# Optimization experiments

Hardware: AMD Instinct MI355X
Metric: run time of the kernel (lower is better)

## Reference

```python
import jax, jax.numpy as jnp
import numpy as np

B, S, D = 4, 2048, 1024
H, HD = 16, 64
DFF = 4096
EPS = 1e-6


def setup_inputs() -> dict:
    key = jax.random.key(0)
    ks = jax.random.split(key, 16)
    sc = 0.02
    def w(k, shape):
        return jax.random.normal(k, shape, dtype=jnp.float32) * sc
    return {
        'x': jax.random.normal(ks[0], (B, S, D), dtype=jnp.float32),
        'wq': w(ks[1], (D, D)), 'bq': jnp.zeros((D,), jnp.float32),
        'wk': w(ks[2], (D, D)), 'bk': jnp.zeros((D,), jnp.float32),
        'wv': w(ks[3], (D, D)), 'bv': jnp.zeros((D,), jnp.float32),
        'wo': w(ks[4], (D, D)), 'bo': jnp.zeros((D,), jnp.float32),
        'w1': w(ks[5], (D, DFF)), 'b1': jnp.zeros((DFF,), jnp.float32),
        'w2': w(ks[6], (DFF, D)), 'b2': jnp.zeros((D,), jnp.float32),
        'ln1_a': jnp.ones((D,), jnp.float32), 'ln1_b': jnp.zeros((D,), jnp.float32),
        'ln2_a': jnp.ones((D,), jnp.float32), 'ln2_b': jnp.zeros((D,), jnp.float32),
    }


def layernorm(x, alpha, bias):
    # Matches torch module: std is unbiased (ddof=1), divide by (std + eps)
    mean = jnp.mean(x, axis=-1, keepdims=True)
    var = jnp.sum((x - mean) ** 2, axis=-1, keepdims=True) / (x.shape[-1] - 1)
    std = jnp.sqrt(var)
    return alpha * ((x - mean) / (std + EPS)) + bias


def mha(x, wq, bq, wk, bk, wv, bv, wo, bo):
    q = (x @ wq + bq).reshape(B, S, H, HD)
    k = (x @ wk + bk).reshape(B, S, H, HD)
    v = (x @ wv + bv).reshape(B, S, H, HD)
    scores = jnp.einsum('bqhd,bkhd->bhqk', q, k) / jnp.sqrt(jnp.float32(HD))
    attn = jax.nn.softmax(scores, axis=-1)
    out = jnp.einsum('bhqk,bkhd->bqhd', attn, v).reshape(B, S, D)
    return out @ wo + bo


def reference(x, wq, bq, wk, bk, wv, bv, wo, bo, w1, b1, w2, b2,
              ln1_a, ln1_b, ln2_a, ln2_b):
    # Residual 1: x + MHA(LN(x))   (dropout = identity, eval mode)
    x = x + mha(layernorm(x, ln1_a, ln1_b), wq, bq, wk, bk, wv, bv, wo, bo)
    # Residual 2: x + FFN(LN(x))
    h = layernorm(x, ln2_a, ln2_b)
    ffn = jax.nn.relu(h @ w1 + b1) @ w2 + b2
    return x + ffn
```

## Files before the change

### kernel.cpp

```cpp
#include <hip/hip_runtime.h>

#define S_ 2048
#define D_ 1024

typedef unsigned short u16;
typedef unsigned int u32;
typedef __bf16 bf16x8 __attribute__((ext_vector_type(8)));
typedef unsigned short us8 __attribute__((ext_vector_type(8)));
typedef unsigned short us4 __attribute__((ext_vector_type(4)));
typedef unsigned int u32x4 __attribute__((ext_vector_type(4)));
typedef float f32x4 __attribute__((ext_vector_type(4)));

#if __has_builtin(__builtin_amdgcn_exp2f)
#define EXP2(x) __builtin_amdgcn_exp2f(x)
#else
#define EXP2(x) exp2f(x)
#endif

static __device__ __forceinline__ u16 f2bf(float f) {
  unsigned u = __builtin_bit_cast(unsigned, f);
  u += 0x7fffu + ((u >> 16) & 1u);
  return (u16)(u >> 16);
}

static __device__ __forceinline__ unsigned cvtpk_bf16(float lo, float hi) {
  unsigned r;
  asm("v_cvt_pk_bf16_f32 %0, %1, %2" : "=v"(r) : "v"(lo), "v"(hi));
  return r;
}

static __device__ __forceinline__ f32x4 mfma16(bf16x8 a, bf16x8 b, f32x4 c) {
  return __builtin_amdgcn_mfma_f32_16x16x32_bf16(a, b, c, 0, 0, 0);
}

static __device__ __forceinline__ void gload16(const void* g, void* lds) {
  __builtin_amdgcn_global_load_lds((const __attribute__((address_space(1))) void*)g,
                                   (__attribute__((address_space(3))) void*)lds, 16, 0, 0);
}

__global__ __launch_bounds__(256) void prep_kernel(
    const float* __restrict__ wq, const float* __restrict__ wk, const float* __restrict__ wv,
    const float* __restrict__ wo, const float* __restrict__ w1, const float* __restrict__ w2,
    const float* __restrict__ bq, const float* __restrict__ bk, const float* __restrict__ bv,
    u16* __restrict__ wqkv, u16* __restrict__ wot, u16* __restrict__ w1t,
    u16* __restrict__ w2t, float* __restrict__ bcat, float qs) {
  const int bid = blockIdx.x;
  const int tx = threadIdx.x, ty = threadIdx.y;
  if (bid >= 12288) {
    const int i = (bid - 12288) * 256 + ty * 32 + tx;
    bcat[i] = (i < 1024) ? bq[i] * qs : ((i < 2048) ? bk[i - 1024] : bv[i - 2048]);
    return;
  }
  const float* in;
  u16* out;
  int K, N, idx;
  float sc = 1.0f;
  if (bid < 4096) {
    K = 1024; N = 1024; idx = bid & 1023;
    if (bid < 1024)      { in = wq; out = wqkv;             sc = qs; }
    else if (bid < 2048) { in = wk; out = wqkv + (1 << 20); }
    else if (bid < 3072) { in = wv; out = wqkv + (2 << 20); }
    else                 { in = wo; out = wot; }
  } else if (bid < 8192) {
    in = w1; out = w1t; K = 1024; N = 4096; idx = bid - 4096;
  } else {
    in = w2; out = w2t; K = 4096; N = 1024; idx = bid - 8192;
  }
  const int nb = N >> 5;
  const int n0 = (idx % nb) * 32, k0 = (idx / nb) * 32;
  __shared__ float t[32][33];
#pragma unroll
  for (int i = 0; i < 4; i++)
    t[ty + 8 * i][tx] = in[(size_t)(k0 + ty + 8 * i) * N + n0 + tx];
  __syncthreads();
#pragma unroll
  for (int i = 0; i < 4; i++)
    out[(size_t)(n0 + ty + 8 * i) * K + k0 + tx] = f2bf(t[tx][ty + 8 * i] * sc);
}

__global__ __launch_bounds__(256) void ln_kernel(const float* __restrict__ in,
                                                 u16* __restrict__ out,
                                                 const float* __restrict__ alpha,
                                                 const float* __restrict__ beta) {
  const int row = blockIdx.x;
  const int tid = threadIdx.x;
  const float4 v = *(const float4*)(in + (size_t)row * D_ + tid * 4);
  float s = v.x + v.y + v.z + v.w;
  float ss = v.x * v.x + v.y * v.y + v.z * v.z + v.w * v.w;
#pragma unroll
  for (int off = 32; off >= 1; off >>= 1) {
    s += __shfl_xor(s, off);
    ss += __shfl_xor(ss, off);
  }
  __shared__ float red[8];
  const int w = tid >> 6, lane = tid & 63;
  if (lane == 0) { red[w] = s; red[4 + w] = ss; }
  __syncthreads();
  s = red[0] + red[1] + red[2] + red[3];
  ss = red[4] + red[5] + red[6] + red[7];
  const float mean = s * (1.0f / D_);
  const float var = (ss - s * mean) * (1.0f / (D_ - 1));
  const float inv = 1.0f / (sqrtf(var) + 1e-6f);
  const int j = tid * 4;
  const float4 av = *(const float4*)(alpha + j);
  const float4 bv = *(const float4*)(beta + j);
  us4 o;
  o[0] = f2bf((v.x - mean) * inv * av.x + bv.x);
  o[1] = f2bf((v.y - mean) * inv * av.y + bv.y);
  o[2] = f2bf((v.z - mean) * inv * av.z + bv.z);
  o[3] = f2bf((v.w - mean) * inv * av.w + bv.w);
  *(us4*)(out + (size_t)row * D_ + j) = o;
}

template <int OM, bool RESID>
__global__ __launch_bounds__(256, 2) void gemm_bt128(const u16* __restrict__ A,
                                                     const u16* __restrict__ Bt,
                                                     const float* __restrict__ bias,
                                                     const float* __restrict__ resid,
                                                     void* __restrict__ outp,
                                                     void* __restrict__ out1,
                                                     void* __restrict__ out2, int N, int K) {
  __shared__ u16 lds[2 * 16384];
  const int tid = threadIdx.x;
  const int lane = tid & 63, w = tid >> 6;
  const int g = lane >> 4, r = lane & 15;
  const int wr = w >> 1, wc = w & 1;
  const int gx = gridDim.x;
  const int nwg = gx * gridDim.y;
  const int orig = blockIdx.y * gx + blockIdx.x;
  const int nid = (orig & 7) * (nwg >> 3) + (orig >> 3);
  const int bx = nid % gx, by = nid / gx;
  const size_t row0 = (size_t)by * 128;
  const int col0 = bx * 128;

  float bias4[4];
#pragma unroll
  for (int n = 0; n < 4; n++) bias4[n] = bias[col0 + wc * 64 + n * 16 + r];

  f32x4 acc[4][4];
#pragma unroll
  for (int m = 0; m < 4; m++)
#pragma unroll
    for (int n = 0; n < 4; n++) {
      f32x4 z = {bias4[n], bias4[n], bias4[n], bias4[n]};
      acc[m][n] = z;
    }

  const int lrow = tid >> 3;
  const int scol = 8 * ((tid & 7) ^ (lrow & 7));
  const u16* gA = A + (row0 + lrow) * (size_t)K + scol;
  const u16* gB = Bt + ((size_t)col0 + lrow) * (size_t)K + scol;
  const int nt = K >> 6;
  const int sw = (r & 7) << 3;

  {
    u16* d = lds + w * 512;
#pragma unroll
    for (int j = 0; j < 4; j++) gload16(gA + (size_t)(j * 32) * K, d + j * 2048);
#pragma unroll
    for (int j = 0; j < 4; j++) gload16(gB + (size_t)(j * 32) * K, d + 8192 + j * 2048);
  }

  for (int t = 0; t < nt; ++t) {
    const u16* As_ = lds + (t & 1) * 16384;
    const u16* Bs_ = As_ + 8192;
    if (t + 1 < nt) {
      u16* d = lds + ((t + 1) & 1) * 16384 + w * 512;
      const size_t ko = (size_t)(t + 1) * 64;
#pragma unroll
      for (int j = 0; j < 4; j++) gload16(gA + (size_t)(j * 32) * K + ko, d + j * 2048);
#pragma unroll
      for (int j = 0; j < 4; j++) gload16(gB + (size_t)(j * 32) * K + ko, d + 8192 + j * 2048);
      asm volatile("s_waitcnt vmcnt(8)" ::: "memory");
    } else {
      asm volatile("s_waitcnt vmcnt(0)" ::: "memory");
    }
    __builtin_amdgcn_s_barrier();
    asm volatile("" ::: "memory");

    bf16x8 bfr[2][4];
#pragma unroll
    for (int kk = 0; kk < 2; kk++)
#pragma unroll
      for (int n = 0; n < 4; n++)
        bfr[kk][n] = __builtin_bit_cast(
            bf16x8, *(const us8*)(Bs_ + (wc * 64 + n * 16 + r) * 64 + ((kk * 32 + g * 8) ^ sw)));

#pragma unroll
    for (int p = 0; p < 4; ++p) {
      const int row = wr * 64 + p * 16 + r;
      bf16x8 a0 = __builtin_bit_cast(bf16x8, *(const us8*)(As_ + row * 64 + ((g * 8) ^ sw)));
      bf16x8 a1 = __builtin_bit_cast(bf16x8, *(const us8*)(As_ + row * 64 + ((32 + g * 8) ^ sw)));
      asm volatile("" ::: "memory");
      if (p > 0) __builtin_amdgcn_s_barrier();
      asm volatile("s_waitcnt lgkmcnt(0)" ::: "memory");
      __builtin_amdgcn_sched_barrier(0);
      __builtin_amdgcn_s_setprio(1);
#pragma unroll
      for (int n = 0; n < 4; n++) {
        acc[p][n] = mfma16(a0, bfr[0][n], acc[p][n]);
        acc[p][n] = mfma16(a1, bfr[1][n], acc[p][n]);
      }
      __builtin_amdgcn_s_setprio(0);
    }
    asm volatile("" ::: "memory");
    __builtin_amdgcn_s_barrier();
  }

#pragma unroll
  for (int m = 0; m < 4; m++)
#pragma unroll
    for (int n = 0; n < 4; n++) {
      if (OM == 2) {
        const int seg = col0 >> 10;
        const int cl = (col0 & 1023) + wc * 64 + n * 16 + r;
        if (seg == 2) {
          const int head = cl >> 6, hd = cl & 63;
          const size_t rg0 = row0 + wr * 64 + m * 16 + 4 * g;
          const int b = (int)(rg0 >> 11), s0 = (int)(rg0 & 2047);
          const int s0p = (s0 & ~63) | (s0 & 32) | ((s0 << 1) & 24) | ((s0 >> 2) & 4);
          us4 o;
#pragma unroll
          for (int i = 0; i < 4; i++) o[i] = f2bf(acc[m][n][i]);
          *(us4*)((u16*)out2 + (((size_t)(b * 16 + head) * 64 + hd) * S_ + s0p)) = o;
        } else {
          u16* dst = (u16*)(seg == 0 ? outp : out1);
#pragma unroll
          for (int i = 0; i < 4; i++) {
            const size_t rg = row0 + wr * 64 + m * 16 + 4 * g + i;
            dst[rg * D_ + cl] = f2bf(acc[m][n][i]);
          }
        }
      } else {
#pragma unroll
        for (int i = 0; i < 4; i++) {
          const size_t rg = row0 + wr * 64 + m * 16 + 4 * g + i;
          const int cg = col0 + wc * 64 + n * 16 + r;
          float v = acc[m][n][i];
          if (RESID) v += resid[rg * N + cg];
          ((float*)outp)[rg * N + cg] = v;
        }
      }
    }
}

template <bool RELU>
__global__ __launch_bounds__(512, 2) void gemm_bt256(const u16* __restrict__ A,
                                                     const u16* __restrict__ Bt,
                                                     const float* __restrict__ bias,
                                                     u16* __restrict__ outp, int N, int K) {
  __shared__ u16 lds[2 * 32768];
  const int tid = threadIdx.x;
  const int lane = tid & 63, w = tid >> 6;
  const int g = lane >> 4, r = lane & 15;
  const int wr = w >> 2, wc = w & 3;
  const int gx = gridDim.x;
  const int nwg = gx * gridDim.y;
  const int orig = blockIdx.y * gx + blockIdx.x;
  const int nid = (orig & 7) * (nwg >> 3) + (orig >> 3);
  const int bx = nid % gx, by = nid / gx;
  const size_t row0 = (size_t)by * 256;
  const int col0 = bx * 256;

  float bias4[4];
#pragma unroll
  for (int n = 0; n < 4; n++) bias4[n] = bias[col0 + wc * 64 + n * 16 + r];

  f32x4 acc[8][4];
#pragma unroll
  for (int m = 0; m < 8; m++)
#pragma unroll
    for (int n = 0; n < 4; n++) {
      f32x4 z = {bias4[n], bias4[n], bias4[n], bias4[n]};
      acc[m][n] = z;
    }

  const int lrow = tid >> 3;
  const int scol = 8 * ((tid & 7) ^ (lrow & 7));
  const u16* gA = A + (row0 + lrow) * (size_t)K + scol;
  const u16* gB = Bt + ((size_t)col0 + lrow) * (size_t)K + scol;
  const int nt = K >> 6;
  const int sw = (r & 7) << 3;

  {
    u16* d = lds + w * 512;
#pragma unroll
    for (int j = 0; j < 4; j++) gload16(gA + (size_t)(j * 64) * K, d + j * 4096);
#pragma unroll
    for (int j = 0; j < 4; j++) gload16(gB + (size_t)(j * 64) * K, d + 16384 + j * 4096);
  }

  for (int t = 0; t < nt; ++t) {
    const u16* As_ = lds + (t & 1) * 32768;
    const u16* Bs_ = As_ + 16384;
    if (t + 1 < nt) {
      u16* d = lds + ((t + 1) & 1) * 32768 + w * 512;
      const size_t ko = (size_t)(t + 1) * 64;
#pragma unroll
      for (int j = 0; j < 4; j++) gload16(gA + (size_t)(j * 64) * K + ko, d + j * 4096);
#pragma unroll
      for (int j = 0; j < 4; j++) gload16(gB + (size_t)(j * 64) * K + ko, d + 16384 + j * 4096);
      asm volatile("s_waitcnt vmcnt(8)" ::: "memory");
    } else {
      asm volatile("s_waitcnt vmcnt(0)" ::: "memory");
    }
    __builtin_amdgcn_s_barrier();
    asm volatile("" ::: "memory");

    bf16x8 bfr[2][4];
#pragma unroll
    for (int kk = 0; kk < 2; kk++)
#pragma unroll
      for (int n = 0; n < 4; n++)
        bfr[kk][n] = __builtin_bit_cast(
            bf16x8, *(const us8*)(Bs_ + (wc * 64 + n * 16 + r) * 64 + ((kk * 32 + g * 8) ^ sw)));

#pragma unroll
    for (int p = 0; p < 4; ++p) {
      bf16x8 af[2][2];
#pragma unroll
      for (int mm = 0; mm < 2; mm++) {
        const int row = wr * 128 + (p * 2 + mm) * 16 + r;
        af[0][mm] = __builtin_bit_cast(bf16x8, *(const us8*)(As_ + row * 64 + ((g * 8) ^ sw)));
        af[1][mm] =
            __builtin_bit_cast(bf16x8, *(const us8*)(As_ + row * 64 + ((32 + g * 8) ^ sw)));
      }
      asm volatile("" ::: "memory");
      if (p > 0) __builtin_amdgcn_s_barrier();
      asm volatile("s_waitcnt lgkmcnt(0)" ::: "memory");
      __builtin_amdgcn_sched_barrier(0);
      __builtin_amdgcn_s_setprio(1);
#pragma unroll
      for (int mm = 0; mm < 2; mm++)
#pragma unroll
        for (int n = 0; n < 4; n++) {
          acc[p * 2 + mm][n] = mfma16(af[0][mm], bfr[0][n], acc[p * 2 + mm][n]);
          acc[p * 2 + mm][n] = mfma16(af[1][mm], bfr[1][n], acc[p * 2 + mm][n]);
        }
      __builtin_amdgcn_s_setprio(0);
    }
    asm volatile("" ::: "memory");
    __builtin_amdgcn_s_barrier();
  }

#pragma unroll
  for (int m = 0; m < 8; m++)
#pragma unroll
    for (int n = 0; n < 4; n++)
#pragma unroll
      for (int i = 0; i < 4; i++) {
        const size_t rg = row0 + wr * 128 + m * 16 + 4 * g + i;
        const int cg = col0 + wc * 64 + n * 16 + r;
        float v = acc[m][n][i];
        if (RELU) v = fmaxf(v, 0.0f);
        outp[rg * N + cg] = f2bf(v);
      }
}

__global__ __launch_bounds__(256) void attn_kernel(const u16* __restrict__ Q,
                                                   const u16* __restrict__ Km,
                                                   const u16* __restrict__ Vt_g,
                                                   u16* __restrict__ O) {
  __shared__ u16 Klds[2 * 4096];
  __shared__ u16 Vlds[2 * 4096];
  const int tid = threadIdx.x;
  const int lane = tid & 63, w = tid >> 6;
  const int g = lane >> 4, r = lane & 15;
  const int orig = blockIdx.y * 16 + blockIdx.x;
  const int nid = (orig & 7) * 128 + (orig >> 3);
  const int qblk = nid & 15, bh = nid >> 4;
  const int b = bh >> 4, head = bh & 15;
  const size_t rowbase = (size_t)b * S_;
  const int colbase = head * 64;
  const int qw = qblk * 128 + w * 32;

  bf16x8 qf0[2], qf1[2];
#pragma unroll
  for (int qh = 0; qh < 2; qh++) {
    const u16* qrow = Q + (rowbase + qw + qh * 16 + r) * D_ + colbase;
    qf0[qh] = __builtin_bit_cast(bf16x8, *(const us8*)(qrow + g * 8));
    qf1[qh] = __builtin_bit_cast(bf16x8, *(const us8*)(qrow + 32 + g * 8));
  }

  const int srow = tid >> 3;
  const int sslot = (tid & 7) ^ (srow & 7);
  const u16* Kg = Km + (rowbase + srow) * D_ + colbase + sslot * 8;
  const u16* Vg = Vt_g + ((size_t)bh * 64 + srow) * S_ + sslot * 8;
  char* lK = (char*)Klds + w * 1024;
  char* lV = (char*)Vlds + w * 1024;

  const us8 onesw = {0x3F80, 0x3F80, 0x3F80, 0x3F80, 0x3F80, 0x3F80, 0x3F80, 0x3F80};
  const bf16x8 ones8 = __builtin_bit_cast(bf16x8, onesw);

  f32x4 lacc[2];
  f32x4 oacc[2][4];
#pragma unroll
  for (int qh = 0; qh < 2; qh++) {
    f32x4 z = {0.0f, 0.0f, 0.0f, 0.0f};
    lacc[qh] = z;
#pragma unroll
    for (int n = 0; n < 4; n++) oacc[qh][n] = z;
  }

  constexpr int NT = S_ / 64;
  gload16(Kg, lK);
  gload16(Kg + (size_t)32 * D_, lK + 4096);
  gload16(Vg, lV);
  gload16(Vg + (size_t)32 * S_, lV + 4096);
  gload16(Kg + (size_t)64 * D_, lK + 8192);
  gload16(Kg + (size_t)96 * D_, lK + 8192 + 4096);
  asm volatile("s_waitcnt vmcnt(2)" ::: "memory");
  __builtin_amdgcn_s_barrier();
  asm volatile("" ::: "memory");

  bf16x8 pa0[2], pa1[2];

  for (int kt = 0; kt < NT; ++kt) {
    const u16* Kc = Klds + (kt & 1) * 4096;
    const u16* Vp = Vlds + ((kt - 1) & 1) * 4096;

    f32x4 st[4][2];
    __builtin_amdgcn_s_setprio(1);
#pragma unroll
    for (int f = 0; f < 4; f++) {
      const int row = f * 16 + r;
      const int sw7 = row & 7;
      const bf16x8 k0 = __builtin_bit_cast(bf16x8, *(const us8*)(Kc + row * 64 + (g ^ sw7) * 8));
      const bf16x8 k1 =
          __builtin_bit_cast(bf16x8, *(const us8*)(Kc + row * 64 + ((g + 4) ^ sw7) * 8));
#pragma unroll
      for (int qh = 0; qh < 2; qh++) {
        f32x4 z = {0.0f, 0.0f, 0.0f, 0.0f};
        st[f][qh] = mfma16(k0, qf0[qh], z);
        st[f][qh] = mfma16(k1, qf1[qh], st[f][qh]);
      }
    }
    __builtin_amdgcn_s_setprio(0);

    if (kt > 0) {
      __builtin_amdgcn_s_setprio(1);
#pragma unroll
      for (int qh = 0; qh < 2; qh++) {
        lacc[qh] = mfma16(pa0[qh], ones8, lacc[qh]);
        lacc[qh] = mfma16(pa1[qh], ones8, lacc[qh]);
      }
#pragma unroll
      for (int n = 0; n < 4; n++) {
        const int row = n * 16 + r;
        const int sw7 = r & 7;
        const bf16x8 vb0 =
            __builtin_bit_cast(bf16x8, *(const us8*)(Vp + row * 64 + (g ^ sw7) * 8));
        const bf16x8 vb1 =
            __builtin_bit_cast(bf16x8, *(const us8*)(Vp + row * 64 + ((4 + g) ^ sw7) * 8));
#pragma unroll
        for (int qh = 0; qh < 2; qh++) {
          oacc[qh][n] = mfma16(pa0[qh], vb0, oacc[qh][n]);
          oacc[qh][n] = mfma16(pa1[qh], vb1, oacc[qh][n]);
        }
      }
      __builtin_amdgcn_s_setprio(0);
    }

    u32 pw[2][8];
#pragma unroll
    for (int qh = 0; qh < 2; qh++)
#pragma unroll
      for (int f = 0; f < 4; f++) {
        const float e0 = EXP2(st[f][qh][0]);
        const float e1 = EXP2(st[f][qh][1]);
        const float e2 = EXP2(st[f][qh][2]);
        const float e3 = EXP2(st[f][qh][3]);
        pw[qh][f * 2] = cvtpk_bf16(e0, e1);
        pw[qh][f * 2 + 1] = cvtpk_bf16(e2, e3);
      }
#pragma unroll
    for (int qh = 0; qh < 2; qh++) {
      const u32x4 a0w = {pw[qh][0], pw[qh][1], pw[qh][2], pw[qh][3]};
      const u32x4 a1w = {pw[qh][4], pw[qh][5], pw[qh][6], pw[qh][7]};
      pa0[qh] = __builtin_bit_cast(bf16x8, a0w);
      pa1[qh] = __builtin_bit_cast(bf16x8, a1w);
    }

    __builtin_amdgcn_s_barrier();
    asm volatile("" ::: "memory");

    if (kt + 2 < NT) {
      gload16(Kg + (size_t)(kt + 2) * 64 * D_, (char*)Klds + (kt & 1) * 8192 + w * 1024);
      gload16(Kg + (size_t)((kt + 2) * 64 + 32) * D_,
              (char*)Klds + (kt & 1) * 8192 + w * 1024 + 4096);
    }
    if (kt + 1 < NT) {
      gload16(Vg + (size_t)(kt + 1) * 64, (char*)Vlds + ((kt + 1) & 1) * 8192 + w * 1024);
      gload16(Vg + (size_t)32 * S_ + (size_t)(kt + 1) * 64,
              (char*)Vlds + ((kt + 1) & 1) * 8192 + w * 1024 + 4096);
    }
    if (kt + 2 < NT)
      asm volatile("s_waitcnt vmcnt(4)" ::: "memory");
    else if (kt + 1 < NT)
      asm volatile("s_waitcnt vmcnt(2)" ::: "memory");
    else
      asm volatile("s_waitcnt vmcnt(0)" ::: "memory");
    __builtin_amdgcn_s_barrier();
    asm volatile("" ::: "memory");
  }

  {
    const u16* Vp = Vlds + ((NT - 1) & 1) * 4096;
#pragma unroll
    for (int qh = 0; qh < 2; qh++) {
      lacc[qh] = mfma16(pa0[qh], ones8, lacc[qh]);
      lacc[qh] = mfma16(pa1[qh], ones8, lacc[qh]);
    }
#pragma unroll
    for (int n = 0; n < 4; n++) {
      const int row = n * 16 + r;
      const int sw7 = r & 7;
      const bf16x8 vb0 = __builtin_bit_cast(bf16x8, *(const us8*)(Vp + row * 64 + (g ^ sw7) * 8));
      const bf16x8 vb1 =
          __builtin_bit_cast(bf16x8, *(const us8*)(Vp + row * 64 + ((4 + g) ^ sw7) * 8));
#pragma unroll
      for (int qh = 0; qh < 2; qh++) {
        oacc[qh][n] = mfma16(pa0[qh], vb0, oacc[qh][n]);
        oacc[qh][n] = mfma16(pa1[qh], vb1, oacc[qh][n]);
      }
    }
  }

#pragma unroll
  for (int qh = 0; qh < 2; qh++) {
    float ld[4];
#pragma unroll
    for (int i = 0; i < 4; i++) ld[i] = 1.0f / lacc[qh][i];
#pragma unroll
    for (int n = 0; n < 4; n++)
#pragma unroll
      for (int i = 0; i < 4; i++)
        O[(rowbase + qw + qh * 16 + 4 * g + i) * D_ + colbase + n * 16 + r] =
            f2bf(oacc[qh][n][i] * ld[i]);
  }
}

extern "C" void kernel_launch(void* const* d_in, const int* in_sizes, int n_in, void* d_out,
                              int out_size, void* d_ws, size_t ws_size, hipStream_t stream) {
  (void)in_sizes; (void)n_in; (void)out_size; (void)ws_size;
  const float* x = (const float*)d_in[0];
  const float* wq = (const float*)d_in[1];
  const float* bq = (const float*)d_in[2];
  const float* wk = (const float*)d_in[3];
  const float* bk = (const float*)d_in[4];
  const float* wv = (const float*)d_in[5];
  const float* bv = (const float*)d_in[6];
  const float* wo = (const float*)d_in[7];
  const float* bo = (const float*)d_in[8];
  const float* w1 = (const float*)d_in[9];
  const float* b1 = (const float*)d_in[10];
  const float* w2 = (const float*)d_in[11];
  const float* b2 = (const float*)d_in[12];
  const float* ln1a = (const float*)d_in[13];
  const float* ln1b = (const float*)d_in[14];
  const float* ln2a = (const float*)d_in[15];
  const float* ln2b = (const float*)d_in[16];

  char* ws = (char*)d_ws;
  const size_t MB = 1ull << 20;
  u16* wqkv = (u16*)(ws + 0 * MB);
  u16* wot = (u16*)(ws + 6 * MB);
  u16* w1t = (u16*)(ws + 8 * MB);
  u16* w2t = (u16*)(ws + 16 * MB);
  u16* xA = (u16*)(ws + 24 * MB);
  u16* qb = (u16*)(ws + 40 * MB);
  u16* kb = (u16*)(ws + 56 * MB);
  u16* vt = (u16*)(ws + 72 * MB);
  float* bcat = (float*)(ws + 88 * MB);
  u16* ff1 = (u16*)(ws + 40 * MB);
  float* x1 = (float*)(ws + 104 * MB);

  const float QSCALE = 0.125f * 1.4426950408889634f;

  prep_kernel<<<12300, dim3(32, 8), 0, stream>>>(wq, wk, wv, wo, w1, w2, bq, bk, bv, wqkv, wot,
                                                 w1t, w2t, bcat, QSCALE);

  ln_kernel<<<8192, 256, 0, stream>>>(x, xA, ln1a, ln1b);
  gemm_bt128<2, false><<<dim3(24, 64), 256, 0, stream>>>(xA, wqkv, bcat, nullptr, qb, kb, vt,
                                                         3072, 1024);
  attn_kernel<<<dim3(16, 64), 256, 0, stream>>>(qb, kb, vt, xA);
  gemm_bt128<1, true><<<dim3(8, 64), 256, 0, stream>>>(xA, wot, bo, x, x1, nullptr, nullptr,
                                                       1024, 1024);
  ln_kernel<<<8192, 256, 0, stream>>>(x1, xA, ln2a, ln2b);
  gemm_bt256<true><<<dim3(16, 32), 512, 0, stream>>>(xA, w1t, b1, ff1, 4096, 1024);
  gemm_bt128<1, true><<<dim3(8, 64), 256, 0, stream>>>(ff1, w2t, b2, x1, (float*)d_out,
                                                       nullptr, nullptr, 1024, 4096);
}
```

Before: 346.8 us.

## Merge LN1 into prep kernel, store residual in bf16, restructure attention pipeline

The first layernorm moves into the weight-prep launch, which removes one kernel launch and lets the LN work overlap with the weight transposes. The post-attention residual x1 is now stored as bf16 instead of fp32, which halves its write traffic and the reads in LN2 and the final GEMM, at some cost in accuracy. The attention kernel now stages K and V in 128-key groups with double buffering and interleaves two 64-key halves per iteration, so fewer barriers are needed per key.

```diff
diff --git a/kernel.cpp b/kernel.cpp
--- a/kernel.cpp
+++ b/kernel.cpp
@@ -23,6 +23,10 @@
   return (u16)(u >> 16);
 }
 
+static __device__ __forceinline__ float bf2f(u16 h) {
+  return __builtin_bit_cast(float, (u32)h << 16);
+}
+
 static __device__ __forceinline__ unsigned cvtpk_bf16(float lo, float hi) {
   unsigned r;
   asm("v_cvt_pk_bf16_f32 %0, %1, %2" : "=v"(r) : "v"(lo), "v"(hi));
@@ -39,32 +43,65 @@
 }
 
 __global__ __launch_bounds__(256) void prep_kernel(
-    const float* __restrict__ wq, const float* __restrict__ wk, const float* __restrict__ wv,
-    const float* __restrict__ wo, const float* __restrict__ w1, const float* __restrict__ w2,
-    const float* __restrict__ bq, const float* __restrict__ bk, const float* __restrict__ bv,
-    u16* __restrict__ wqkv, u16* __restrict__ wot, u16* __restrict__ w1t,
-    u16* __restrict__ w2t, float* __restrict__ bcat, float qs) {
+    const float* __restrict__ x, u16* __restrict__ xA, const float* __restrict__ ln1a,
+    const float* __restrict__ ln1b, const float* __restrict__ wq, const float* __restrict__ wk,
+    const float* __restrict__ wv, const float* __restrict__ wo, const float* __restrict__ w1,
+    const float* __restrict__ w2, const float* __restrict__ bq, const float* __restrict__ bk,
+    const float* __restrict__ bv, u16* __restrict__ wqkv, u16* __restrict__ wot,
+    u16* __restrict__ w1t, u16* __restrict__ w2t, float* __restrict__ bcat, float qs) {
   const int bid = blockIdx.x;
   const int tx = threadIdx.x, ty = threadIdx.y;
-  if (bid >= 12288) {
-    const int i = (bid - 12288) * 256 + ty * 32 + tx;
+  const int tid = ty * 32 + tx;
+  if (bid < 8192) {
+    const int row = bid;
+    const float4 v = *(const float4*)(x + (size_t)row * D_ + tid * 4);
+    float s = v.x + v.y + v.z + v.w;
+    float ss = v.x * v.x + v.y * v.y + v.z * v.z + v.w * v.w;
+#pragma unroll
+    for (int off = 32; off >= 1; off >>= 1) {
+      s += __shfl_xor(s, off);
+      ss += __shfl_xor(ss, off);
+    }
+    __shared__ float red[8];
+    const int w = tid >> 6, lane = tid & 63;
+    if (lane == 0) { red[w] = s; red[4 + w] = ss; }
+    __syncthreads();
+    s = red[0] + red[1] + red[2] + red[3];
+    ss = red[4] + red[5] + red[6] + red[7];
+    const float mean = s * (1.0f / D_);
+    const float var = (ss - s * mean) * (1.0f / (D_ - 1));
+    const float inv = 1.0f / (sqrtf(var) + 1e-6f);
+    const int j = tid * 4;
+    const float4 av = *(const float4*)(ln1a + j);
+    const float4 bv = *(const float4*)(ln1b + j);
+    us4 o;
+    o[0] = f2bf((v.x - mean) * inv * av.x + bv.x);
+    o[1] = f2bf((v.y - mean) * inv * av.y + bv.y);
+    o[2] = f2bf((v.z - mean) * inv * av.z + bv.z);
+    o[3] = f2bf((v.w - mean) * inv * av.w + bv.w);
+    *(us4*)(xA + (size_t)row * D_ + j) = o;
+    return;
+  }
+  if (bid >= 20480) {
+    const int i = (bid - 20480) * 256 + tid;
     bcat[i] = (i < 1024) ? bq[i] * qs : ((i < 2048) ? bk[i - 1024] : bv[i - 2048]);
     return;
   }
+  const int tb = bid - 8192;
   const float* in;
   u16* out;
   int K, N, idx;
   float sc = 1.0f;
-  if (bid < 4096) {
-    K = 1024; N = 1024; idx = bid & 1023;
-    if (bid < 1024)      { in = wq; out = wqkv;             sc = qs; }
-    else if (bid < 2048) { in = wk; out = wqkv + (1 << 20); }
-    else if (bid < 3072) { in = wv; out = wqkv + (2 << 20); }
-    else                 { in = wo; out = wot; }
-  } else if (bid < 8192) {
-    in = w1; out = w1t; K = 1024; N = 4096; idx = bid - 4096;
+  if (tb < 4096) {
+    K = 1024; N = 1024; idx = tb & 1023;
+    if (tb < 1024)      { in = wq; out = wqkv;             sc = qs; }
+    else if (tb < 2048) { in = wk; out = wqkv + (1 << 20); }
+    else if (tb < 3072) { in = wv; out = wqkv + (2 << 20); }
+    else                { in = wo; out = wot; }
+  } else if (tb < 8192) {
+    in = w1; out = w1t; K = 1024; N = 4096; idx = tb - 4096;
   } else {
-    in = w2; out = w2t; K = 4096; N = 1024; idx = bid - 8192;
+    in = w2; out = w2t; K = 4096; N = 1024; idx = tb - 8192;
   }
   const int nb = N >> 5;
   const int n0 = (idx % nb) * 32, k0 = (idx / nb) * 32;
@@ -78,15 +115,16 @@
     out[(size_t)(n0 + ty + 8 * i) * K + k0 + tx] = f2bf(t[tx][ty + 8 * i] * sc);
 }
 
-__global__ __launch_bounds__(256) void ln_kernel(const float* __restrict__ in,
-                                                 u16* __restrict__ out,
-                                                 const float* __restrict__ alpha,
-                                                 const float* __restrict__ beta) {
+__global__ __launch_bounds__(256) void ln_bf16_kernel(const u16* __restrict__ in,
+                                                      u16* __restrict__ out,
+                                                      const float* __restrict__ alpha,
+                                                      const float* __restrict__ beta) {
   const int row = blockIdx.x;
   const int tid = threadIdx.x;
-  const float4 v = *(const float4*)(in + (size_t)row * D_ + tid * 4);
-  float s = v.x + v.y + v.z + v.w;
-  float ss = v.x * v.x + v.y * v.y + v.z * v.z + v.w * v.w;
+  const us4 h = *(const us4*)(in + (size_t)row * D_ + tid * 4);
+  float v0 = bf2f(h[0]), v1 = bf2f(h[1]), v2 = bf2f(h[2]), v3 = bf2f(h[3]);
+  float s = v0 + v1 + v2 + v3;
+  float ss = v0 * v0 + v1 * v1 + v2 * v2 + v3 * v3;
 #pragma unroll
   for (int off = 32; off >= 1; off >>= 1) {
     s += __shfl_xor(s, off);
@@ -105,18 +143,18 @@
   const float4 av = *(const float4*)(alpha + j);
   const float4 bv = *(const float4*)(beta + j);
   us4 o;
-  o[0] = f2bf((v.x - mean) * inv * av.x + bv.x);
-  o[1] = f2bf((v.y - mean) * inv * av.y + bv.y);
-  o[2] = f2bf((v.z - mean) * inv * av.z + bv.z);
-  o[3] = f2bf((v.w - mean) * inv * av.w + bv.w);
+  o[0] = f2bf((v0 - mean) * inv * av.x + bv.x);
+  o[1] = f2bf((v1 - mean) * inv * av.y + bv.y);
+  o[2] = f2bf((v2 - mean) * inv * av.z + bv.z);
+  o[3] = f2bf((v3 - mean) * inv * av.w + bv.w);
   *(us4*)(out + (size_t)row * D_ + j) = o;
 }
 
-template <int OM, bool RESID>
+template <int OM, int RESID>
 __global__ __launch_bounds__(256, 2) void gemm_bt128(const u16* __restrict__ A,
                                                      const u16* __restrict__ Bt,
                                                      const float* __restrict__ bias,
-                                                     const float* __restrict__ resid,
+                                                     const void* __restrict__ resid,
                                                      void* __restrict__ outp,
                                                      void* __restrict__ out1,
                                                      void* __restrict__ out2, int N, int K) {
@@ -237,8 +275,12 @@
           const size_t rg = row0 + wr * 64 + m * 16 + 4 * g + i;
           const int cg = col0 + wc * 64 + n * 16 + r;
           float v = acc[m][n][i];
-          if (RESID) v += resid[rg * N + cg];
-          ((float*)outp)[rg * N + cg] = v;
+          if (RESID == 1) v += ((const float*)resid)[rg * N + cg];
+          if (RESID == 2) v += bf2f(((const u16*)resid)[rg * N + cg]);
+          if (OM == 1)
+            ((float*)outp)[rg * N + cg] = v;
+          else
+            ((u16*)outp)[rg * N + cg] = f2bf(v);
         }
       }
     }
@@ -361,8 +403,8 @@
                                                    const u16* __restrict__ Km,
                                                    const u16* __restrict__ Vt_g,
                                                    u16* __restrict__ O) {
-  __shared__ u16 Klds[2 * 4096];
-  __shared__ u16 Vlds[2 * 4096];
+  __shared__ u16 Klds[2][2][4096];
+  __shared__ u16 Vlds[2][2][4096];
   const int tid = threadIdx.x;
   const int lane = tid & 63, w = tid >> 6;
   const int g = lane >> 4, r = lane & 15;
@@ -386,8 +428,6 @@
   const int sslot = (tid & 7) ^ (srow & 7);
   const u16* Kg = Km + (rowbase + srow) * D_ + colbase + sslot * 8;
   const u16* Vg = Vt_g + ((size_t)bh * 64 + srow) * S_ + sslot * 8;
-  char* lK = (char*)Klds + w * 1024;
-  char* lV = (char*)Vlds + w * 1024;
 
   const us8 onesw = {0x3F80, 0x3F80, 0x3F80, 0x3F80, 0x3F80, 0x3F80, 0x3F80, 0x3F80};
   const bf16x8 ones8 = __builtin_bit_cast(bf16x8, onesw);
@@ -402,129 +442,152 @@
     for (int n = 0; n < 4; n++) oacc[qh][n] = z;
   }
 
-  constexpr int NT = S_ / 64;
-  gload16(Kg, lK);
-  gload16(Kg + (size_t)32 * D_, lK + 4096);
-  gload16(Vg, lV);
-  gload16(Vg + (size_t)32 * S_, lV + 4096);
-  gload16(Kg + (size_t)64 * D_, lK + 8192);
-  gload16(Kg + (size_t)96 * D_, lK + 8192 + 4096);
-  asm volatile("s_waitcnt vmcnt(2)" ::: "memory");
-  __builtin_amdgcn_s_barrier();
-  asm volatile("" ::: "memory");
-
-  bf16x8 pa0[2], pa1[2];
-
-  for (int kt = 0; kt < NT; ++kt) {
-    const u16* Kc = Klds + (kt & 1) * 4096;
-    const u16* Vp = Vlds + ((kt - 1) & 1) * 4096;
-
-    f32x4 st[4][2];
+  constexpr int NG = S_ / 128;
+
+#define STAGE_GRP(t, bq_)                                                              \
+  {                                                                                    \
+    const int _t = (t), _b = (bq_);                                                    \
+    _Pragma("unroll") for (int h = 0; h < 2; h++) {                                    \
+      gload16(Kg + (size_t)(_t * 128 + h * 64) * D_, (char*)&Klds[_b][h][0] + w * 1024); \
+      gload16(Kg + (size_t)(_t * 128 + h * 64 + 32) * D_,                              \
+              (char*)&Klds[_b][h][0] + w * 1024 + 4096);                               \
+      gload16(Vg + _t * 128 + h * 64, (char*)&Vlds[_b][h][0] + w * 1024);              \
+      gload16(Vg + (size_t)32 * S_ + _t * 128 + h * 64,                                \
+              (char*)&Vlds[_b][h][0] + w * 1024 + 4096);                               \
+    }                                                                                  \
+  }
+
+  STAGE_GRP(0, 0);
+
+  for (int t = 0; t < NG; ++t) {
+    const int buf = t & 1;
+    if (t + 1 < NG) {
+      STAGE_GRP(t + 1, buf ^ 1);
+      asm volatile("s_waitcnt vmcnt(8)" ::: "memory");
+    } else {
+      asm volatile("s_waitcnt vmcnt(0)" ::: "memory");
+    }
+    __builtin_amdgcn_s_barrier();
+    asm volatile("" ::: "memory");
+
+    f32x4 st0[4][2];
     __builtin_amdgcn_s_setprio(1);
 #pragma unroll
     for (int f = 0; f < 4; f++) {
       const int row = f * 16 + r;
       const int sw7 = row & 7;
+      const u16* Kc = &Klds[buf][0][0];
       const bf16x8 k0 = __builtin_bit_cast(bf16x8, *(const us8*)(Kc + row * 64 + (g ^ sw7) * 8));
       const bf16x8 k1 =
           __builtin_bit_cast(bf16x8, *(const us8*)(Kc + row * 64 + ((g + 4) ^ sw7) * 8));
 #pragma unroll
       for (int qh = 0; qh < 2; qh++) {
         f32x4 z = {0.0f, 0.0f, 0.0f, 0.0f};
-        st[f][qh] = mfma16(k0, qf0[qh], z);
-        st[f][qh] = mfma16(k1, qf1[qh], st[f][qh]);
+        st0[f][qh] = mfma16(k0, qf0[qh], z);
+        st0[f][qh] = mfma16(k1, qf1[qh], st0[f][qh]);
       }
     }
     __builtin_amdgcn_s_setprio(0);
-
-    if (kt > 0) {
-      __builtin_amdgcn_s_setprio(1);
+    bf16x8 paA0[2], paA1[2];
+#pragma unroll
+    for (int qh = 0; qh < 2; qh++) {
+      u32 pw[8];
+#pragma unroll
+      for (int f = 0; f < 4; f++) {
+        const float e0 = EXP2(st0[f][qh][0]);
+        const float e1 = EXP2(st0[f][qh][1]);
+        const float e2 = EXP2(st0[f][qh][2]);
+        const float e3 = EXP2(st0[f][qh][3]);
+        pw[f * 2] = cvtpk_bf16(e0, e1);
+        pw[f * 2 + 1] = cvtpk_bf16(e2, e3);
+      }
+      const u32x4 a0w = {pw[0], pw[1], pw[2], pw[3]};
+      const u32x4 a1w = {pw[4], pw[5], pw[6], pw[7]};
+      paA0[qh] = __builtin_bit_cast(bf16x8, a0w);
+      paA1[qh] = __builtin_bit_cast(bf16x8, a1w);
+    }
+    f32x4 st1[4][2];
+    __builtin_amdgcn_s_setprio(1);
+#pragma unroll
+    for (int f = 0; f < 4; f++) {
+      const int row = f * 16 + r;
+      const int sw7 = row & 7;
+      const u16* Kc = &Klds[buf][1][0];
+      const bf16x8 k0 = __builtin_bit_cast(bf16x8, *(const us8*)(Kc + row * 64 + (g ^ sw7) * 8));
+      const bf16x8 k1 =
+          __builtin_bit_cast(bf16x8, *(const us8*)(Kc + row * 64 + ((g + 4) ^ sw7) * 8));
 #pragma unroll
       for (int qh = 0; qh < 2; qh++) {
-        lacc[qh] = mfma16(pa0[qh], ones8, lacc[qh]);
-        lacc[qh] = mfma16(pa1[qh], ones8, lacc[qh]);
-      }
-#pragma unroll
-      for (int n = 0; n < 4; n++) {
-        const int row = n * 16 + r;
-        const int sw7 = r & 7;
-        const bf16x8 vb0 =
-            __builtin_bit_cast(bf16x8, *(const us8*)(Vp + row * 64 + (g ^ sw7) * 8));
-        const bf16x8 vb1 =
-            __builtin_bit_cast(bf16x8, *(const us8*)(Vp + row * 64 + ((4 + g) ^ sw7) * 8));
-#pragma unroll
-        for (int qh = 0; qh < 2; qh++) {
-          oacc[qh][n] = mfma16(pa0[qh], vb0, oacc[qh][n]);
-          oacc[qh][n] = mfma16(pa1[qh], vb1, oacc[qh][n]);
-        }
-      }
-      __builtin_amdgcn_s_setprio(0);
-    }
-
-    u32 pw[2][8];
-#pragma unroll
-    for (int qh = 0; qh < 2; qh++)
-#pragma unroll
-      for (int f = 0; f < 4; f++) {
-        const float e0 = EXP2(st[f][qh][0]);
-        const float e1 = EXP2(st[f][qh][1]);
-        const float e2 = EXP2(st[f][qh][2]);
-        const float e3 = EXP2(st[f][qh][3]);
-        pw[qh][f * 2] = cvtpk_bf16(e0, e1);
-        pw[qh][f * 2 + 1] = cvtpk_bf16(e2, e3);
-      }
+        f32x4 z = {0.0f, 0.0f, 0.0f, 0.0f};
+        st1[f][qh] = mfma16(k0, qf0[qh], z);
+        st1[f][qh] = mfma16(k1, qf1[qh], st1[f][qh]);
+      }
+    }
 #pragma unroll
     for (int qh = 0; qh < 2; qh++) {
-      const u32x4 a0w = {pw[qh][0], pw[qh][1], pw[qh][2], pw[qh][3]};
-      const u32x4 a1w = {pw[qh][4], pw[qh][5], pw[qh][6], pw[qh][7]};
-      pa0[qh] = __builtin_bit_cast(bf16x8, a0w);
-      pa1[qh] = __builtin_bit_cast(bf16x8, a1w);
-    }
-
-    __builtin_amdgcn_s_barrier();
-    asm volatile("" ::: "memory");
-
-    if (kt + 2 < NT) {
-      gload16(Kg + (size_t)(kt + 2) * 64 * D_, (char*)Klds + (kt & 1) * 8192 + w * 1024);
-      gload16(Kg + (size_t)((kt + 2) * 64 + 32) * D_,
-              (char*)Klds + (kt & 1) * 8192 + w * 1024 + 4096);
-    }
-    if (kt + 1 < NT) {
-      gload16(Vg + (size_t)(kt + 1) * 64, (char*)Vlds + ((kt + 1) & 1) * 8192 + w * 1024);
-      gload16(Vg + (size_t)32 * S_ + (size_t)(kt + 1) * 64,
-              (char*)Vlds + ((kt + 1) & 1) * 8192 + w * 1024 + 4096);
-    }
-    if (kt + 2 < NT)
-      asm volatile("s_waitcnt vmcnt(4)" ::: "memory");
-    else if (kt + 1 < NT)
-      asm volatile("s_waitcnt vmcnt(2)" ::: "memory");
-    else
-      asm volatile("s_waitcnt vmcnt(0)" ::: "memory");
-    __builtin_amdgcn_s_barrier();
-    asm volatile("" ::: "memory");
-  }
-
-  {
-    const u16* Vp = Vlds + ((NT - 1) & 1) * 4096;
-#pragma unroll
-    for (int qh = 0; qh < 2; qh++) {
-      lacc[qh] = mfma16(pa0[qh], ones8, lacc[qh]);
-      lacc[qh] = mfma16(pa1[qh], ones8, lacc[qh]);
+      lacc[qh] = mfma16(paA0[qh], ones8, lacc[qh]);
+      lacc[qh] = mfma16(paA1[qh], ones8, lacc[qh]);
     }
 #pragma unroll
     for (int n = 0; n < 4; n++) {
       const int row = n * 16 + r;
       const int sw7 = r & 7;
-      const bf16x8 vb0 = __builtin_bit_cast(bf16x8, *(const us8*)(Vp + row * 64 + (g ^ sw7) * 8));
+      const u16* Vc = &Vlds[buf][0][0];
+      const bf16x8 vb0 = __builtin_bit_cast(bf16x8, *(const us8*)(Vc + row * 64 + (g ^ sw7) * 8));
       const bf16x8 vb1 =
-          __builtin_bit_cast(bf16x8, *(const us8*)(Vp + row * 64 + ((4 + g) ^ sw7) * 8));
+          __builtin_bit_cast(bf16x8, *(const us8*)(Vc + row * 64 + ((4 + g) ^ sw7) * 8));
 #pragma unroll
       for (int qh = 0; qh < 2; qh++) {
-        oacc[qh][n] = mfma16(pa0[qh], vb0, oacc[qh][n]);
-        oacc[qh][n] = mfma16(pa1[qh], vb1, oacc[qh][n]);
-      }
-    }
-  }
+        oacc[qh][n] = mfma16(paA0[qh], vb0, oacc[qh][n]);
+        oacc[qh][n] = mfma16(paA1[qh], vb1, oacc[qh][n]);
+      }
+    }
+    __builtin_amdgcn_s_setprio(0);
+    bf16x8 paB0[2], paB1[2];
+#pragma unroll
+    for (int qh = 0; qh < 2; qh++) {
+      u32 pw[8];
+#pragma unroll
+      for (int f = 0; f < 4; f++) {
+        const float e0 = EXP2(st1[f][qh][0]);
+        const float e1 = EXP2(st1[f][qh][1]);
+        const float e2 = EXP2(st1[f][qh][2]);
+        const float e3 = EXP2(st1[f][qh][3]);
+        pw[f * 2] = cvtpk_bf16(e0, e1);
+        pw[f * 2 + 1] = cvtpk_bf16(e2, e3);
+      }
+      const u32x4 a0w = {pw[0], pw[1], pw[2], pw[3]};
+      const u32x4 a1w = {pw[4], pw[5], pw[6], pw[7]};
+      paB0[qh] = __builtin_bit_cast(bf16x8, a0w);
+      paB1[qh] = __builtin_bit_cast(bf16x8, a1w);
+    }
+    __builtin_amdgcn_s_setprio(1);
+#pragma unroll
+    for (int qh = 0; qh < 2; qh++) {
+      lacc[qh] = mfma16(paB0[qh], ones8, lacc[qh]);
+      lacc[qh] = mfma16(paB1[qh], ones8, lacc[qh]);
+    }
+#pragma unroll
+    for (int n = 0; n < 4; n++) {
+      const int row = n * 16 + r;
+      const int sw7 = r & 7;
+      const u16* Vc = &Vlds[buf][1][0];
+      const bf16x8 vb0 = __builtin_bit_cast(bf16x8, *(const us8*)(Vc + row * 64 + (g ^ sw7) * 8));
+      const bf16x8 vb1 =
+          __builtin_bit_cast(bf16x8, *(const us8*)(Vc + row * 64 + ((4 + g) ^ sw7) * 8));
+#pragma unroll
+      for (int qh = 0; qh < 2; qh++) {
+        oacc[qh][n] = mfma16(paB0[qh], vb0, oacc[qh][n]);
+        oacc[qh][n] = mfma16(paB1[qh], vb1, oacc[qh][n]);
+      }
+    }
+    __builtin_amdgcn_s_setprio(0);
+
+    asm volatile("" ::: "memory");
+    __builtin_amdgcn_s_barrier();
+    asm volatile("" ::: "memory");
+  }
+#undef STAGE_GRP
 
 #pragma unroll
   for (int qh = 0; qh < 2; qh++) {
@@ -573,21 +636,19 @@
   u16* vt = (u16*)(ws + 72 * MB);
   float* bcat = (float*)(ws + 88 * MB);
   u16* ff1 = (u16*)(ws + 40 * MB);
-  float* x1 = (float*)(ws + 104 * MB);
+  u16* x1b = (u16*)(ws + 104 * MB);
 
   const float QSCALE = 0.125f * 1.4426950408889634f;
 
-  prep_kernel<<<12300, dim3(32, 8), 0, stream>>>(wq, wk, wv, wo, w1, w2, bq, bk, bv, wqkv, wot,
-                                                 w1t, w2t, bcat, QSCALE);
-
-  ln_kernel<<<8192, 256, 0, stream>>>(x, xA, ln1a, ln1b);
-  gemm_bt128<2, false><<<dim3(24, 64), 256, 0, stream>>>(xA, wqkv, bcat, nullptr, qb, kb, vt,
-                                                         3072, 1024);
+  prep_kernel<<<20492, dim3(32, 8), 0, stream>>>(x, xA, ln1a, ln1b, wq, wk, wv, wo, w1, w2, bq,
+                                                 bk, bv, wqkv, wot, w1t, w2t, bcat, QSCALE);
+  gemm_bt128<2, 0><<<dim3(24, 64), 256, 0, stream>>>(xA, wqkv, bcat, nullptr, qb, kb, vt, 3072,
+                                                     1024);
   attn_kernel<<<dim3(16, 64), 256, 0, stream>>>(qb, kb, vt, xA);
-  gemm_bt128<1, true><<<dim3(8, 64), 256, 0, stream>>>(xA, wot, bo, x, x1, nullptr, nullptr,
-                                                       1024, 1024);
-  ln_kernel<<<8192, 256, 0, stream>>>(x1, xA, ln2a, ln2b);
+  gemm_bt128<0, 1><<<dim3(8, 64), 256, 0, stream>>>(xA, wot, bo, x, x1b, nullptr, nullptr, 1024,
+                                                    1024);
+  ln_bf16_kernel<<<8192, 256, 0, stream>>>(x1b, xA, ln2a, ln2b);
   gemm_bt256<true><<<dim3(16, 32), 512, 0, stream>>>(xA, w1t, b1, ff1, 4096, 1024);
-  gemm_bt128<1, true><<<dim3(8, 64), 256, 0, stream>>>(ff1, w2t, b2, x1, (float*)d_out,
-                                                       nullptr, nullptr, 1024, 4096);
-}
+  gemm_bt128<1, 2><<<dim3(8, 64), 256, 0, stream>>>(ff1, w2t, b2, x1b, (float*)d_out, nullptr,
+                                                    nullptr, 1024, 4096);
+}
```

Result: faster. 333.0 us (-4.0%).
